# Optimization experiments

Measured on AMD Instinct MI355X. Metric: run time of the kernel, lower is better.

Reference implementation:

```python
import jax, jax.numpy as jnp
import numpy as np

N_EMBD = 1024
N_HEAD = 16
B, L = 2, 2048


def setup_inputs() -> dict:
    key = jax.random.key(0)
    k1, k2, k3, k4 = jax.random.split(key, 4)
    x = jax.random.normal(k1, (B, L, N_EMBD), dtype=jnp.float32)
    W_qkv = jax.random.normal(k2, (N_EMBD, 3 * N_EMBD), dtype=jnp.float32) * 0.02
    b_qkv = jnp.zeros((3 * N_EMBD,), dtype=jnp.float32)
    W_o = jax.random.normal(k3, (N_EMBD, N_EMBD), dtype=jnp.float32) * 0.02
    b_o = jnp.zeros((N_EMBD,), dtype=jnp.float32)
    mask_len = jax.random.randint(k4, (B,), 1, L, dtype=jnp.int32)
    return {"x": x, "W_qkv": W_qkv, "b_qkv": b_qkv, "W_o": W_o, "b_o": b_o,
            "mask_len": mask_len}


def reference(x, W_qkv, b_qkv, W_o, b_o, mask_len):
    Bx, Lx, E = x.shape
    H = N_HEAD
    D = E // H
    # causal mask [1,1,L,L]; then zero out query rows i >= mask_len[b]
    mask = jnp.tri(Lx)[None, None, :, :]
    row_invalid = jnp.arange(Lx).reshape(1, 1, Lx, 1) >= mask_len.reshape(Bx, 1, 1, 1)
    mask = jnp.where(row_invalid, 0.0, mask)  # [B,1,L,L]
    # QKV projection; note original packs per-head 3D-chunks: reshape (B,L,H,3D)
    h = x @ W_qkv + b_qkv                      # [B,L,3E]
    h = h.reshape(Bx, Lx, H, 3 * D).transpose(0, 2, 1, 3)  # [B,H,L,3D]
    q, k, v = jnp.split(h, 3, axis=-1)         # each [B,H,L,D]
    attn = jnp.einsum('bhqd,bhkd->bhqk', q, k) / jnp.sqrt(jnp.float32(D))
    attn = jnp.where(mask == 0, -1e18, attn)
    attn = jax.nn.softmax(attn, axis=-1)
    # dropout: deterministic (train=False) -> identity
    y = jnp.einsum('bhqk,bhkd->bhqd', attn, v)  # [B,H,L,D]
    y = y.transpose(0, 2, 1, 3).reshape(Bx, Lx, E)
    return y @ W_o + b_o
```

## Files before the change

kernel.cpp:

```cpp
#include <hip/hip_runtime.h>

typedef unsigned short u16;
typedef unsigned int u32;
typedef __bf16 bf16x8 __attribute__((ext_vector_type(8)));
typedef float f32x4 __attribute__((ext_vector_type(4)));
typedef u16 u16x4 __attribute__((ext_vector_type(4)));
typedef u16 u16x8 __attribute__((ext_vector_type(8)));

#define LSEQ 2048
#define EMB  1024
#define NH   16
#define HDIM 64

#define QSCALE 0.1803368808f

#if __has_builtin(__builtin_amdgcn_exp2f)
#define EXP2(x) __builtin_amdgcn_exp2f(x)
#else
#define EXP2(x) __expf((x) * 0.6931471805599453f)
#endif

__device__ __forceinline__ u16 cvt_bf(float f) {
  __bf16 h = (__bf16)f;
  return __builtin_bit_cast(u16, h);
}
__device__ __forceinline__ float bf2f(u16 v) {
  return __uint_as_float(((unsigned)v) << 16);
}
__device__ __forceinline__ void async16(void* lds, const void* g) {
  __builtin_amdgcn_global_load_lds((const __attribute__((address_space(1))) void*)g,
                                   (__attribute__((address_space(3))) void*)lds, 16, 0, 0);
}
__device__ __forceinline__ f32x4 mfma16(bf16x8 a, bf16x8 b, f32x4 c) {
  return __builtin_amdgcn_mfma_f32_16x16x32_bf16(a, b, c, 0, 0, 0);
}

__global__ void prep(const float* __restrict__ x, u16* __restrict__ xb,
                     const float* __restrict__ Wqkv, u16* __restrict__ WqkvT,
                     const float* __restrict__ Wo, u16* __restrict__ WoT) {
  __shared__ float tile[32][33];
  const int bid = blockIdx.x;
  const int tid = threadIdx.x;
  if (bid < 2048) {
    const int n4 = 1024 * 1024;
    for (int i = bid * 256 + tid; i < n4; i += 2048 * 256) {
      float4 v = ((const float4*)x)[i];
      u16x4 o = { cvt_bf(v.x), cvt_bf(v.y), cvt_bf(v.z), cvt_bf(v.w) };
      ((u16x4*)xb)[i] = o;
    }
    return;
  }
  const int idx = bid - 2048;
  const int bx = idx & 127, by = idx >> 7;
  const int Kd = 1024;
  const float* in;
  u16* out;
  int Nd, n0;
  if (bx < 96) { in = Wqkv; out = WqkvT; Nd = 3072; n0 = bx * 32; }
  else         { in = Wo;   out = WoT;   Nd = 1024; n0 = (bx - 96) * 32; }
  const int k0 = by * 32;
  const int tx = tid & 31, ty = tid >> 5;
#pragma unroll
  for (int i = 0; i < 4; ++i)
    tile[ty + i * 8][tx] = in[(size_t)(k0 + ty + i * 8) * Nd + n0 + tx];
  __syncthreads();
#pragma unroll
  for (int i = 0; i < 4; ++i)
    out[(size_t)(n0 + ty + i * 8) * Kd + k0 + tx] = cvt_bf(tile[tx][ty + i * 8]);
}

__launch_bounds__(256, 2)
__global__ void gemm_qkv(const u16* __restrict__ A, const u16* __restrict__ Bt,
                         const float* __restrict__ bias,
                         u16* __restrict__ Qo, u16* __restrict__ Ko, u16* __restrict__ Vo,
                         const int* __restrict__ mask_len) {
  __shared__ __attribute__((aligned(16))) u16 SMEM[4 * 8192];
  u16* As = SMEM;
  u16* Bs = SMEM + 2 * 8192;
  const int tid = threadIdx.x;
  const int w = tid >> 6, l = tid & 63;
  const int g = l >> 4, cc = l & 15;
  const int orig = blockIdx.y * 24 + blockIdx.x;
  const int wgid = (orig & 7) * 96 + (orig >> 3);
  const int m0 = (wgid / 24) * 128;
  const int tb = wgid % 24;
  const int type = tb >> 3, tbh = tb & 7;
  const int bb = m0 >> 11;
  const int lo = mask_len[bb];
  if (type < 2 && (m0 & (LSEQ - 1)) >= lo) return;
  const int wm = w >> 1, wn = w & 1;
  const int K = 1024;

  const int srow8 = tid >> 3;
  const int chunk = tid & 7;
  auto stage = [&](int buf, int k0) {
#pragma unroll
    for (int c = 0; c < 4; ++c) {
      int R = c * 32 + srow8;
      int col = (chunk ^ (R & 7)) * 8;
      async16((char*)&As[buf * 8192] + c * 4096 + w * 1024,
              A + (size_t)(m0 + R) * K + k0 + col);
      int gR = (2 * tbh + (R >> 6)) * 192 + type * 64 + (R & 63);
      async16((char*)&Bs[buf * 8192] + c * 4096 + w * 1024,
              Bt + (size_t)gR * K + k0 + col);
    }
  };

  f32x4 acc[4][4] = {};
  stage(0, 0);
  for (int t = 0; t < 16; ++t) {
    const int cur = t & 1;
    if (t + 1 < 16) {
      stage(cur ^ 1, (t + 1) * 64);
      asm volatile("s_waitcnt vmcnt(8)" ::: "memory");
    } else {
      asm volatile("s_waitcnt vmcnt(0)" ::: "memory");
    }
    __builtin_amdgcn_s_barrier();
    __builtin_amdgcn_sched_barrier(0);
    const char* AB = (const char*)&As[cur * 8192];
    const char* BB = (const char*)&Bs[cur * 8192];
#pragma unroll
    for (int ks = 0; ks < 2; ++ks) {
      bf16x8 af[4], bfr[4];
#pragma unroll
      for (int mf = 0; mf < 4; ++mf) {
        int row = wm * 64 + mf * 16 + cc;
        af[mf] = *(const bf16x8*)(AB + row * 128 + ((ks * 64 + g * 16) ^ ((row & 7) << 4)));
      }
#pragma unroll
      for (int nf = 0; nf < 4; ++nf) {
        int row = wn * 64 + nf * 16 + cc;
        bfr[nf] = *(const bf16x8*)(BB + row * 128 + ((ks * 64 + g * 16) ^ ((row & 7) << 4)));
      }
#pragma unroll
      for (int mf = 0; mf < 4; ++mf)
#pragma unroll
        for (int nf = 0; nf < 4; ++nf)
          acc[mf][nf] = mfma16(af[mf], bfr[nf], acc[mf][nf]);
    }
    __builtin_amdgcn_s_barrier();
  }

  __syncthreads();
  {
    char* P = (char*)SMEM + wn * 16384;
    const float* bptr = bias + (2 * tbh + wn) * 192 + type * 64;
#pragma unroll
    for (int mf = 0; mf < 4; ++mf) {
#pragma unroll
      for (int nf = 0; nf < 4; ++nf) {
        int d = nf * 16 + cc;
        float bv = bptr[d];
#pragma unroll
        for (int r = 0; r < 4; ++r) {
          int ml = wm * 64 + mf * 16 + g * 4 + r;
          float val = acc[mf][nf][r] + bv;
          if (type == 0) val *= QSCALE;
          u16 hv = cvt_bf(val);
          if (type == 2) *(u16*)(P + d * 256 + ((ml * 2) ^ ((d & 7) << 5))) = hv;
          else           *(u16*)(P + ml * 128 + ((d * 2) ^ (((ml >> 2) & 3) << 5))) = hv;
        }
      }
    }
  }
  __syncthreads();
  const int ls0 = m0 & (LSEQ - 1);
#pragma unroll
  for (int wi = 0; wi < 2; ++wi) {
    const int bh = bb * NH + 2 * tbh + wi;
    char* P = (char*)SMEM + wi * 16384;
    if (type == 2) {
      u16* dstb = Vo + (size_t)bh * HDIM * LSEQ + ls0;
#pragma unroll
      for (int it = 0; it < 4; ++it) {
        int idx = it * 256 + tid;
        int row = idx >> 4;
        int colB = (idx & 15) * 16;
        int4 v = *(const int4*)(P + row * 256 + (colB ^ ((row & 7) << 5)));
        *(int4*)((char*)(dstb + (size_t)row * LSEQ) + colB) = v;
      }
    } else {
      u16* dst = (type == 0 ? Qo : Ko) + ((size_t)bh * LSEQ + ls0) * HDIM;
#pragma unroll
      for (int it = 0; it < 4; ++it) {
        int idx = it * 256 + tid;
        int row = idx >> 3;
        int colB = (idx & 7) * 16;
        int4 v = *(const int4*)(P + row * 128 + (colB ^ (((row >> 2) & 3) << 5)));
        *(int4*)((char*)dst + row * 128 + colB) = v;
      }
    }
  }
}

template<int NCOLS, int BM>
__launch_bounds__(256)
__global__ void gemm_out(const u16* __restrict__ A, const u16* __restrict__ Bt,
                         const float* __restrict__ bias, float* __restrict__ Out) {
  constexpr int MF = BM / 32;
  constexpr int ABUF = BM * 32;
  __shared__ __attribute__((aligned(16))) u16 SMEM[3 * ABUF + 3 * 128 * 32];
  u16* As = SMEM;
  u16* Bs = SMEM + 3 * ABUF;
  const int tid = threadIdx.x;
  const int w = tid >> 6, l = tid & 63;
  const int g = l >> 4, cc = l & 15;
  constexpr int GX = NCOLS / 128;
  constexpr int NWG = (4096 / BM) * GX;
  constexpr int CPX = NWG / 8;
  const int orig = blockIdx.y * GX + blockIdx.x;
  const int wgid = (orig & 7) * CPX + (orig >> 3);
  const int m0 = (wgid / GX) * BM, n0 = (wgid % GX) * 128;
  const int wm = w >> 1, wn = w & 1;
  const int K = 1024;
  const int srow = tid >> 2;
  const int scol = (tid & 3) * 8;
  const u16* Ag = A + (size_t)(m0 + srow) * K + scol;
  const u16* Bg0 = Bt + (size_t)(n0 + srow) * K + scol;
  const u16* Bg1 = Bt + (size_t)(n0 + srow + 64) * K + scol;
  f32x4 acc[MF][4] = {};

  auto stage = [&](int buf, int k0) {
    async16(&As[buf * ABUF + w * 512], Ag + k0);
    async16(&Bs[buf * 4096 + w * 512], Bg0 + k0);
    async16(&Bs[buf * 4096 + 2048 + w * 512], Bg1 + k0);
  };

  stage(0, 0);
  stage(1, 32);
  int buf = 0;
  for (int k0 = 0; k0 < K; k0 += 32) {
    if (k0 + 32 < K) asm volatile("s_waitcnt vmcnt(3)" ::: "memory");
    else             asm volatile("s_waitcnt vmcnt(0)" ::: "memory");
    __builtin_amdgcn_s_barrier();
    __builtin_amdgcn_sched_barrier(0);
    if (k0 + 64 < K) {
      int nb = buf + 2; if (nb >= 3) nb -= 3;
      stage(nb, k0 + 64);
    }
    bf16x8 af[MF], bfr[4];
#pragma unroll
    for (int mf = 0; mf < MF; ++mf)
      af[mf] = *(const bf16x8*)&As[buf * ABUF + (wm * (BM / 2) + mf * 16 + cc) * 32 + g * 8];
#pragma unroll
    for (int nf = 0; nf < 4; ++nf)
      bfr[nf] = *(const bf16x8*)&Bs[buf * 4096 + (wn * 64 + nf * 16 + cc) * 32 + g * 8];
#pragma unroll
    for (int mf = 0; mf < MF; ++mf)
#pragma unroll
      for (int nf = 0; nf < 4; ++nf)
        acc[mf][nf] = mfma16(af[mf], bfr[nf], acc[mf][nf]);
    if (++buf == 3) buf = 0;
  }

#pragma unroll
  for (int mf = 0; mf < MF; ++mf) {
#pragma unroll
    for (int nf = 0; nf < 4; ++nf) {
      int n = n0 + wn * 64 + nf * 16 + cc;
      float bv = bias[n];
#pragma unroll
      for (int r = 0; r < 4; ++r) {
        int m = m0 + wm * (BM / 2) + mf * 16 + g * 4 + r;
        Out[(size_t)m * NCOLS + n] = acc[mf][nf][r] + bv;
      }
    }
  }
}

__launch_bounds__(256)
__global__ void attn_fwd(const u16* __restrict__ Q, const u16* __restrict__ Kb,
                         const u16* __restrict__ Vt, const int* __restrict__ mask_len,
                         u16* __restrict__ Y) {
  __shared__ __attribute__((aligned(16))) u16 Ks[2][64 * 64];
  __shared__ __attribute__((aligned(16))) u16 Vs[2][64 * 64];
  __shared__ __attribute__((aligned(16))) u16 Ps[4 * 16 * 64];
  const int tid = threadIdx.x;
  const int i = blockIdx.x;

  if (i >= 1024) {
    float* partial = (float*)Ks;
    u16* mv = (u16*)((char*)Ks + 1024);
    int bh = i - 1024, b = bh >> 4, h = bh & (NH - 1);
    int d = tid >> 2, part = tid & 3;
    const u16* src = Vt + ((size_t)bh * HDIM + d) * LSEQ + part * 512;
    float s = 0.f;
    for (int ii = 0; ii < 512; ii += 8) {
      u16x8 v = *(const u16x8*)&src[ii];
#pragma unroll
      for (int jj = 0; jj < 8; ++jj) s += bf2f(v[jj]);
    }
    partial[tid] = s;
    __syncthreads();
    if (part == 0) {
      float t = partial[tid] + partial[tid + 1] + partial[tid + 2] + partial[tid + 3];
      mv[d] = cvt_bf(t * (1.0f / (float)LSEQ));
    }
    __syncthreads();
    int lo = mask_len[b];
    if (lo < 0) lo = 0;
    if (lo > LSEQ) lo = LSEQ;
    int total = (LSEQ - lo) * HDIM;
    for (int idx = tid; idx < total; idx += 256) {
      int row = lo + (idx >> 6), dd = idx & 63;
      Y[((size_t)b * LSEQ + row) * EMB + h * HDIM + dd] = mv[dd];
    }
    return;
  }

  const int w = tid >> 6, l = tid & 63;
  const int g = l >> 4, cc = l & 15;
  const int bh = i & 31;
  const int k = i >> 5, grp = k >> 3, j = k & 7;
  int qblk;
  if (grp == 0) qblk = 31 - j;
  else if (grp == 1) qblk = j;
  else if (grp == 2) qblk = 23 - j;
  else qblk = 8 + j;
  const int q0 = qblk * 64;
  const int nt = qblk + 1;
  const int b = bh >> 4, h = bh & (NH - 1);

  const int lo = mask_len[b];
  if (q0 >= lo) return;

  const int sr = w * 8 + (l >> 3);
  const int pb = (l & 7) * 16;
  char* Pw = (char*)&Ps[w * 16 * 64];
  const int xc = (cc & 7) << 4;

  auto stageKV = [&](int buf, int t) {
    const int kv0 = t * 64;
#pragma unroll
    for (int ch = 0; ch < 2; ++ch) {
      int R = sr + ch * 32;
      int dcol = (pb ^ ((R & 7) << 4)) >> 1;
      async16((char*)Ks[buf] + ch * 4096 + w * 1024,
              Kb + ((size_t)bh * LSEQ + kv0 + R) * HDIM + dcol);
      async16((char*)Vs[buf] + ch * 4096 + w * 1024,
              Vt + ((size_t)bh * HDIM + R) * LSEQ + kv0 + dcol);
    }
  };

  const u16* Qg = Q + ((size_t)bh * LSEQ + q0 + w * 16) * HDIM;
  bf16x8 qf0 = *(const bf16x8*)&Qg[cc * HDIM + g * 8];
  bf16x8 qf1 = *(const bf16x8*)&Qg[cc * HDIM + 32 + g * 8];

  bf16x8 onesf;
#pragma unroll
  for (int z = 0; z < 8; ++z) onesf[z] = (__bf16)1.0f;

  f32x4 o[4] = {};
  f32x4 ls = {};

  stageKV(0, 0);

  for (int t = 0; t < nt; ++t) {
    const int cur = t & 1;
    if (t + 1 < nt) {
      stageKV(cur ^ 1, t + 1);
      asm volatile("s_waitcnt vmcnt(4)" ::: "memory");
    } else {
      asm volatile("s_waitcnt vmcnt(0)" ::: "memory");
    }
    __builtin_amdgcn_s_barrier();
    __builtin_amdgcn_sched_barrier(0);
    const char* KsB = (const char*)Ks[cur];
    const char* VsB = (const char*)Vs[cur];

    f32x4 sf[4] = {};
    __builtin_amdgcn_s_setprio(1);
#pragma unroll
    for (int nf = 0; nf < 4; ++nf) {
      bf16x8 kf0 = *(const bf16x8*)(KsB + (nf * 16 + cc) * 128 + ((g * 16) ^ xc));
      bf16x8 kf1 = *(const bf16x8*)(KsB + (nf * 16 + cc) * 128 + ((64 + g * 16) ^ xc));
      sf[nf] = mfma16(qf0, kf0, sf[nf]);
      sf[nf] = mfma16(qf1, kf1, sf[nf]);
    }
    __builtin_amdgcn_s_setprio(0);

    if (t == nt - 1) {
#pragma unroll
      for (int nf = 0; nf < 4; ++nf) {
        int kvl = nf * 16 + cc;
#pragma unroll
        for (int r = 0; r < 4; ++r)
          if (kvl > w * 16 + g * 4 + r) sf[nf][r] = -1e30f;
      }
    }

#pragma unroll
    for (int r = 0; r < 4; ++r) {
      int q = g * 4 + r;
      int xr = (q & 7) << 4;
#pragma unroll
      for (int nf = 0; nf < 4; ++nf) {
        float pv = EXP2(sf[nf][r]);
        *(u16*)(Pw + q * 128 + (((nf * 16 + cc) * 2) ^ xr)) = cvt_bf(pv);
      }
    }
    asm volatile("s_waitcnt lgkmcnt(0)" ::: "memory");
    __builtin_amdgcn_sched_barrier(0);

    bf16x8 pf0 = *(const bf16x8*)(Pw + cc * 128 + ((g * 16) ^ xc));
    bf16x8 pf1 = *(const bf16x8*)(Pw + cc * 128 + ((64 + g * 16) ^ xc));
    __builtin_amdgcn_s_setprio(1);
    ls = mfma16(pf1, onesf, mfma16(pf0, onesf, ls));
#pragma unroll
    for (int nf = 0; nf < 4; ++nf) {
      bf16x8 vf0 = *(const bf16x8*)(VsB + (nf * 16 + cc) * 128 + ((g * 16) ^ xc));
      bf16x8 vf1 = *(const bf16x8*)(VsB + (nf * 16 + cc) * 128 + ((64 + g * 16) ^ xc));
      o[nf] = mfma16(pf0, vf0, o[nf]);
      o[nf] = mfma16(pf1, vf1, o[nf]);
    }
    __builtin_amdgcn_s_setprio(0);
    __builtin_amdgcn_s_barrier();
  }

#pragma unroll
  for (int r = 0; r < 4; ++r) {
    int row = q0 + w * 16 + g * 4 + r;
    if (row < lo) {
      float inv = 1.0f / ls[r];
      size_t base = ((size_t)b * LSEQ + row) * EMB + h * HDIM;
#pragma unroll
      for (int nf = 0; nf < 4; ++nf)
        Y[base + nf * 16 + cc] = cvt_bf(o[nf][r] * inv);
    }
  }
}

extern "C" void kernel_launch(void* const* d_in, const int* in_sizes, int n_in,
                              void* d_out, int out_size, void* d_ws, size_t ws_size,
                              hipStream_t stream) {
  (void)in_sizes; (void)n_in; (void)out_size; (void)ws_size;
  const float* x    = (const float*)d_in[0];
  const float* Wqkv = (const float*)d_in[1];
  const float* bqkv = (const float*)d_in[2];
  const float* Wo   = (const float*)d_in[3];
  const float* bo   = (const float*)d_in[4];
  const int* mask_len = (const int*)d_in[5];
  float* out = (float*)d_out;

  u16* ws = (u16*)d_ws;
  u16* xb    = ws;
  u16* wqkvt = ws + (size_t)4 * 1024 * 1024;
  u16* wot   = wqkvt + (size_t)3 * 1024 * 1024;
  u16* Qb    = wot + (size_t)1024 * 1024;
  u16* Kb    = Qb + (size_t)4 * 1024 * 1024;
  u16* Vtb   = Kb + (size_t)4 * 1024 * 1024;
  u16* Yb    = xb;

  prep<<<6144, 256, 0, stream>>>(x, xb, Wqkv, wqkvt, Wo, wot);
  gemm_qkv<<<dim3(24, 32), 256, 0, stream>>>(xb, wqkvt, bqkv, Qb, Kb, Vtb, mask_len);
  attn_fwd<<<1056, 256, 0, stream>>>(Qb, Kb, Vtb, mask_len, Yb);
  gemm_out<1024, 64><<<dim3(8, 64), 256, 0, stream>>>(Yb, wot, bo, out);
}
```

Measured before the change: 94.40 us.

## Skip output GEMM tiles for masked rows; compute constant row via mean-V GEMV

Masked query rows all produce the same output: the mean of V projected through W_o. The attention kernel now writes only the per-batch mean-V vector instead of filling Y rows. The output GEMM skips whole M tiles beyond mask_len and guards per-row stores. Extra blocks compute mean-V times W_o plus bias once and broadcast it to the masked rows. This removes GEMM work and Y writes in proportion to the masked fraction, at the cost of a small GEMV and some broadcast stores.

After: 105.5 us. 11.7% more time.

```diff
diff --git a/kernel.cpp b/kernel.cpp
--- a/kernel.cpp
+++ b/kernel.cpp
@@ -197,21 +197,53 @@
 template<int NCOLS, int BM>
 __launch_bounds__(256)
 __global__ void gemm_out(const u16* __restrict__ A, const u16* __restrict__ Bt,
-                         const float* __restrict__ bias, float* __restrict__ Out) {
+                         const float* __restrict__ bias, float* __restrict__ Out,
+                         const u16* __restrict__ mvY, const int* __restrict__ mask_len) {
   constexpr int MF = BM / 32;
   constexpr int ABUF = BM * 32;
   __shared__ __attribute__((aligned(16))) u16 SMEM[3 * ABUF + 3 * 128 * 32];
   u16* As = SMEM;
   u16* Bs = SMEM + 3 * ABUF;
   const int tid = threadIdx.x;
+  const int orig = blockIdx.y * 8 + blockIdx.x;
+
+  if (orig >= 512) {
+    const int sb = orig - 512;
+    const int b = sb >> 3, n0 = (sb & 7) * 128;
+    int lo = mask_len[b];
+    if (lo < 0) lo = 0;
+    if (lo >= LSEQ) return;
+    float* mrow = (float*)SMEM;
+    const int j = tid >> 1, half = tid & 1;
+    const u16* wrow = Bt + (size_t)(n0 + j) * 1024 + half * 512;
+    const u16* mvp = mvY + (size_t)b * EMB + half * 512;
+    float s = 0.f;
+    for (int k = 0; k < 512; k += 8) {
+      u16x8 a = *(const u16x8*)&mvp[k];
+      u16x8 wv = *(const u16x8*)&wrow[k];
+#pragma unroll
+      for (int z = 0; z < 8; ++z) s += bf2f(a[z]) * bf2f(wv[z]);
+    }
+    s += __shfl_xor(s, 1);
+    if (half == 0) mrow[j] = s + bias[n0 + j];
+    __syncthreads();
+    float4 v = *(const float4*)&mrow[(tid & 31) * 4];
+    for (int row = lo + (tid >> 5); row < LSEQ; row += 8)
+      *(float4*)&Out[((size_t)b * LSEQ + row) * NCOLS + n0 + (tid & 31) * 4] = v;
+    return;
+  }
+
   const int w = tid >> 6, l = tid & 63;
   const int g = l >> 4, cc = l & 15;
   constexpr int GX = NCOLS / 128;
   constexpr int NWG = (4096 / BM) * GX;
   constexpr int CPX = NWG / 8;
-  const int orig = blockIdx.y * GX + blockIdx.x;
   const int wgid = (orig & 7) * CPX + (orig >> 3);
   const int m0 = (wgid / GX) * BM, n0 = (wgid % GX) * 128;
+  const int bb = m0 >> 11;
+  int lo = mask_len[bb];
+  if (lo < 0) lo = 0;
+  if ((m0 & (LSEQ - 1)) >= lo) return;
   const int wm = w >> 1, wn = w & 1;
   const int K = 1024;
   const int srow = tid >> 2;
@@ -263,7 +295,8 @@
 #pragma unroll
       for (int r = 0; r < 4; ++r) {
         int m = m0 + wm * (BM / 2) + mf * 16 + g * 4 + r;
-        Out[(size_t)m * NCOLS + n] = acc[mf][nf][r] + bv;
+        if ((m & (LSEQ - 1)) < lo)
+          Out[(size_t)m * NCOLS + n] = acc[mf][nf][r] + bv;
       }
     }
   }
@@ -272,7 +305,7 @@
 __launch_bounds__(256)
 __global__ void attn_fwd(const u16* __restrict__ Q, const u16* __restrict__ Kb,
                          const u16* __restrict__ Vt, const int* __restrict__ mask_len,
-                         u16* __restrict__ Y) {
+                         u16* __restrict__ Y, u16* __restrict__ mvY) {
   __shared__ __attribute__((aligned(16))) u16 Ks[2][64 * 64];
   __shared__ __attribute__((aligned(16))) u16 Vs[2][64 * 64];
   __shared__ __attribute__((aligned(16))) u16 Ps[4 * 16 * 64];
@@ -281,7 +314,6 @@
 
   if (i >= 1024) {
     float* partial = (float*)Ks;
-    u16* mv = (u16*)((char*)Ks + 1024);
     int bh = i - 1024, b = bh >> 4, h = bh & (NH - 1);
     int d = tid >> 2, part = tid & 3;
     const u16* src = Vt + ((size_t)bh * HDIM + d) * LSEQ + part * 512;
@@ -295,16 +327,7 @@
     __syncthreads();
     if (part == 0) {
       float t = partial[tid] + partial[tid + 1] + partial[tid + 2] + partial[tid + 3];
-      mv[d] = cvt_bf(t * (1.0f / (float)LSEQ));
-    }
-    __syncthreads();
-    int lo = mask_len[b];
-    if (lo < 0) lo = 0;
-    if (lo > LSEQ) lo = LSEQ;
-    int total = (LSEQ - lo) * HDIM;
-    for (int idx = tid; idx < total; idx += 256) {
-      int row = lo + (idx >> 6), dd = idx & 63;
-      Y[((size_t)b * LSEQ + row) * EMB + h * HDIM + dd] = mv[dd];
+      mvY[(size_t)b * EMB + h * HDIM + d] = cvt_bf(t * (1.0f / (float)LSEQ));
     }
     return;
   }
@@ -450,10 +473,11 @@
   u16* Qb    = wot + (size_t)1024 * 1024;
   u16* Kb    = Qb + (size_t)4 * 1024 * 1024;
   u16* Vtb   = Kb + (size_t)4 * 1024 * 1024;
+  u16* mvYb  = Vtb + (size_t)4 * 1024 * 1024;
   u16* Yb    = xb;
 
   prep<<<6144, 256, 0, stream>>>(x, xb, Wqkv, wqkvt, Wo, wot);
   gemm_qkv<<<dim3(24, 32), 256, 0, stream>>>(xb, wqkvt, bqkv, Qb, Kb, Vtb, mask_len);
-  attn_fwd<<<1056, 256, 0, stream>>>(Qb, Kb, Vtb, mask_len, Yb);
-  gemm_out<1024, 64><<<dim3(8, 64), 256, 0, stream>>>(Yb, wot, bo, out);
-}
+  attn_fwd<<<1056, 256, 0, stream>>>(Qb, Kb, Vtb, mask_len, Yb, mvYb);
+  gemm_out<1024, 64><<<dim3(8, 66), 256, 0, stream>>>(Yb, wot, bo, out, mvYb, mask_len);
+}
```
